# Kernel tuning notes

Hardware: AMD Instinct MI355X
Metric: run time of the kernel (lower is better)

Reference implementation:

```python
import jax, jax.numpy as jnp
import numpy as np

T, B, E, H = 2048, 2, 1024, 16
D = E // H  # head_dim = 64


def setup_inputs() -> dict:
    key = jax.random.key(0)
    ks = jax.random.split(key, 5)
    s = 1.0 / np.sqrt(E)  # keep projections well-scaled like xavier init
    return {
        "query": jax.random.normal(ks[0], (T, B, E), jnp.float32),
        "Wq": jax.random.normal(ks[1], (E, E), jnp.float32) * s,
        "bq": jnp.zeros((E,), jnp.float32),
        "Wk": jax.random.normal(ks[2], (E, E), jnp.float32) * s,
        "bk": jnp.zeros((E,), jnp.float32),
        "Wv": jax.random.normal(ks[3], (E, E), jnp.float32) * s,
        "bv": jnp.zeros((E,), jnp.float32),
        "Wo": jax.random.normal(ks[4], (E, E), jnp.float32) * s,
        "bo": jnp.zeros((E,), jnp.float32),
    }


def reference(query, Wq, bq, Wk, bk, Wv, bv, Wo, bo):
    # query: [T, B, E] (seq_len, batch, embed_dim), fairseq layout
    scaling = D ** -0.5
    q = (query @ Wq.T + bq) * scaling           # [T, B, E]
    k = query @ Wk.T + bk                       # [T, B, E] (self-attention)
    v = query @ Wv.T + bv                       # [T, B, E]
    # split heads: [T, B, H, D]
    q = q.reshape(T, B, H, D)
    k = k.reshape(T, B, H, D)
    v = v.reshape(T, B, H, D)
    # attention scores [B, H, T, S] (S == T, no masks, global window)
    scores = jnp.einsum("tbhd,sbhd->bhts", q, k)
    probs = jax.nn.softmax(scores, axis=-1)     # dropout p=0 -> identity
    attn = jnp.einsum("bhts,sbhd->tbhd", probs, v).reshape(T, B, E)
    return attn @ Wo.T + bo                     # [T, B, E]
```

## Files before the change

### kernel.cpp

```cpp
#include <hip/hip_runtime.h>
#include <hip/hip_bf16.h>
#include <stdint.h>


#define T_SEQ 2048
#define BATCH 2
#define EMB   1024
#define NH    16
#define HD    64

typedef short s16;
typedef s16   bf16x8 __attribute__((ext_vector_type(8)));
typedef float f32x4  __attribute__((ext_vector_type(4)));

__device__ __forceinline__ f32x4 mfma16(bf16x8 a, bf16x8 b, f32x4 c) {
  return __builtin_amdgcn_mfma_f32_16x16x32_bf16(a, b, c, 0, 0, 0);
}

__device__ __forceinline__ void gload16(const void* g, void* l) {
  __builtin_amdgcn_global_load_lds(
      (const __attribute__((address_space(1))) uint32_t*)g,
      (__attribute__((address_space(3))) uint32_t*)l, 16, 0, 0);
}

__device__ __forceinline__ s16 f2b(float x) {
  return (s16)__builtin_bit_cast(unsigned short, __float2bfloat16(x));
}
__device__ __forceinline__ uint32_t pack2(float lo, float hi) {
  return ((uint32_t)(uint16_t)__builtin_bit_cast(unsigned short, __float2bfloat16(hi)) << 16)
       |  (uint32_t)(uint16_t)__builtin_bit_cast(unsigned short, __float2bfloat16(lo));
}

__device__ __forceinline__ bf16x8 cvt8(const float* p) {
  f32x4 a = *(const f32x4*)p;
  f32x4 b = *(const f32x4*)(p + 4);
  bf16x8 r;
  r[0] = f2b(a[0]); r[1] = f2b(a[1]); r[2] = f2b(a[2]); r[3] = f2b(a[3]);
  r[4] = f2b(b[0]); r[5] = f2b(b[1]); r[6] = f2b(b[2]); r[7] = f2b(b[3]);
  return r;
}

__global__ __launch_bounds__(256)
void gemm_qkv_kernel(const float* __restrict__ X,
                     const float* __restrict__ Wq, const float* __restrict__ bq,
                     const float* __restrict__ Wk, const float* __restrict__ bk,
                     const float* __restrict__ Wv, const float* __restrict__ bv,
                     __hip_bfloat16* __restrict__ Qh, __hip_bfloat16* __restrict__ Kh,
                     s16* __restrict__ Vt)
{
  __shared__ __align__(16) s16 lA[128 * 32];
  __shared__ __align__(16) s16 lB[128 * 32];
  const int tid  = threadIdx.x;
  const int lane = tid & 63;
  const int wave = tid >> 6;
  const int which = blockIdx.y >> 3;
  const float* W = (which == 0) ? Wq : (which == 1) ? Wk : Wv;
  const float* bias = (which == 0) ? bq : (which == 1) ? bk : bv;
  const int m0 = blockIdx.x * 128;
  const int n0 = (blockIdx.y & 7) * 128;
  const int srow = tid >> 2;
  const int scol = (tid & 3) * 8;
  const int wr = (wave >> 1) * 64;
  const int wc = (wave & 1) * 64;
  const int fr = lane & 15;
  const int fk = (lane >> 4) * 8;

  f32x4 acc[4][4] = {};

  for (int k0 = 0; k0 < EMB; k0 += 32) {
    bf16x8 a0 = cvt8(X + (size_t)(m0 + srow) * EMB + k0 + scol);
    bf16x8 a1 = cvt8(X + (size_t)(m0 + 64 + srow) * EMB + k0 + scol);
    bf16x8 b0 = cvt8(W + (size_t)(n0 + srow) * EMB + k0 + scol);
    bf16x8 b1 = cvt8(W + (size_t)(n0 + 64 + srow) * EMB + k0 + scol);
    *(bf16x8*)&lA[srow * 32 + scol] = a0;
    *(bf16x8*)&lA[(64 + srow) * 32 + scol] = a1;
    *(bf16x8*)&lB[srow * 32 + scol] = b0;
    *(bf16x8*)&lB[(64 + srow) * 32 + scol] = b1;
    __syncthreads();
    bf16x8 af[4], bfr[4];
#pragma unroll
    for (int i = 0; i < 4; ++i) af[i]  = *(const bf16x8*)&lA[(wr + i * 16 + fr) * 32 + fk];
#pragma unroll
    for (int i = 0; i < 4; ++i) bfr[i] = *(const bf16x8*)&lB[(wc + i * 16 + fr) * 32 + fk];
#pragma unroll
    for (int mi = 0; mi < 4; ++mi)
#pragma unroll
      for (int ni = 0; ni < 4; ++ni)
        acc[mi][ni] = mfma16(af[mi], bfr[ni], acc[mi][ni]);
    __syncthreads();
  }

  const float scale = (which == 0) ? 0.125f * 1.44269504088896f : 1.0f;
  __hip_bfloat16* Y = (which == 0) ? Qh : Kh;
  const int fq = lane >> 4;
#pragma unroll
  for (int mi = 0; mi < 4; ++mi) {
#pragma unroll
    for (int ni = 0; ni < 4; ++ni) {
      const int nn = n0 + wc + ni * 16 + fr;
      const float bb = bias[nn];
      const int h = nn >> 6, d = nn & 63;
#pragma unroll
      for (int r = 0; r < 4; ++r) {
        const int m = m0 + wr + mi * 16 + fq * 4 + r;
        const int t = m >> 1, b = m & 1;
        const float y = (acc[mi][ni][r] + bb) * scale;
        if (which == 2) {
          const int tl = t & 31;
          const int tp = ((tl & 12) << 1) + (tl & 3) + ((tl >> 4) << 2);
          Vt[(((size_t)b * NH + h) * HD + d) * T_SEQ + (t & ~31) + tp] = f2b(y);
        } else {
          Y[(((size_t)b * NH + h) * T_SEQ + t) * HD + d] = __float2bfloat16(y);
        }
      }
    }
  }
}

__global__ __launch_bounds__(256)
void gemm_out_kernel(const s16* __restrict__ X,
                     const float* __restrict__ W,
                     const float* __restrict__ bias,
                     float* __restrict__ Y)
{
  __shared__ __align__(16) s16 lA[128 * 32];
  __shared__ __align__(16) s16 lB[128 * 32];
  const int tid  = threadIdx.x;
  const int lane = tid & 63;
  const int wave = tid >> 6;
  const int m0 = blockIdx.x * 128;
  const int n0 = blockIdx.y * 128;
  const int srow = tid >> 2;
  const int scol = (tid & 3) * 8;
  const int wr = (wave >> 1) * 64;
  const int wc = (wave & 1) * 64;
  const int fr = lane & 15;
  const int fk = (lane >> 4) * 8;

  f32x4 acc[4][4] = {};

  for (int k0 = 0; k0 < EMB; k0 += 32) {
    gload16(X + (size_t)(m0 + srow) * EMB + k0 + scol,      &lA[srow * 32 + scol]);
    gload16(X + (size_t)(m0 + 64 + srow) * EMB + k0 + scol, &lA[(64 + srow) * 32 + scol]);
    bf16x8 b0 = cvt8(W + (size_t)(n0 + srow) * EMB + k0 + scol);
    bf16x8 b1 = cvt8(W + (size_t)(n0 + 64 + srow) * EMB + k0 + scol);
    *(bf16x8*)&lB[srow * 32 + scol] = b0;
    *(bf16x8*)&lB[(64 + srow) * 32 + scol] = b1;
    __syncthreads();
    bf16x8 af[4], bfr[4];
#pragma unroll
    for (int i = 0; i < 4; ++i) af[i]  = *(const bf16x8*)&lA[(wr + i * 16 + fr) * 32 + fk];
#pragma unroll
    for (int i = 0; i < 4; ++i) bfr[i] = *(const bf16x8*)&lB[(wc + i * 16 + fr) * 32 + fk];
#pragma unroll
    for (int mi = 0; mi < 4; ++mi)
#pragma unroll
      for (int ni = 0; ni < 4; ++ni)
        acc[mi][ni] = mfma16(af[mi], bfr[ni], acc[mi][ni]);
    __syncthreads();
  }

  const int fq = lane >> 4;
#pragma unroll
  for (int mi = 0; mi < 4; ++mi) {
#pragma unroll
    for (int ni = 0; ni < 4; ++ni) {
      const int nn = n0 + wc + ni * 16 + fr;
      const float bb = bias[nn];
#pragma unroll
      for (int r = 0; r < 4; ++r) {
        const int m = m0 + wr + mi * 16 + fq * 4 + r;
        Y[(size_t)m * EMB + nn] = acc[mi][ni][r] + bb;
      }
    }
  }
}

__global__ __launch_bounds__(256, 4)
void attn_kernel(const s16* __restrict__ Qh,
                 const s16* __restrict__ Kh,
                 const s16* __restrict__ Vt,
                 __hip_bfloat16* __restrict__ attn)
{
  __shared__ __align__(16) s16 lK[2][64 * 64];
  __shared__ __align__(16) s16 lV[2][64 * 64];
  const int tid  = threadIdx.x;
  const int lane = tid & 63;
  const int wave = tid >> 6;

  const int lid = blockIdx.x;
  const int nid = (lid & 7) * 128 + (lid >> 3);
  const int qb = nid & 31;
  const int bh = nid >> 5;

  const int q0 = qb * 64 + wave * 16;
  const size_t baseK = (size_t)bh * T_SEQ * HD;
  const size_t baseV = (size_t)bh * HD * T_SEQ;
  const int fr = lane & 15;
  const int fq = lane >> 4;
  const int fk = fq * 8;
  const int xk = fr & 7;

  const int srow  = tid >> 3;
  const int scol  = (tid & 7) * 8;
  const int scolK = (((tid & 7) ^ ((tid >> 3) & 7)) * 8);

  const bf16x8 qf0 = *(const bf16x8*)&Qh[baseK + (size_t)(q0 + fr) * HD + fk];
  const bf16x8 qf1 = *(const bf16x8*)&Qh[baseK + (size_t)(q0 + fr) * HD + 32 + fk];

  float m_run = -INFINITY, l_run = 0.f;
  f32x4 o_acc[4] = {};

  auto stage = [&](int b, int sB) {
    gload16(Kh + baseK + (size_t)(sB + srow) * HD + scolK,         &lK[b][srow * 64 + scol]);
    gload16(Kh + baseK + (size_t)(sB + 32 + srow) * HD + scolK,    &lK[b][(32 + srow) * 64 + scol]);
    gload16(Vt + baseV + (size_t)srow * T_SEQ + sB + scolK,        &lV[b][srow * 64 + scol]);
    gload16(Vt + baseV + (size_t)(32 + srow) * T_SEQ + sB + scolK, &lV[b][(32 + srow) * 64 + scol]);
  };

  stage(0, 0);

  for (int t = 0; t < T_SEQ / 64; ++t) {
    const int cur = t & 1;
    __syncthreads();
    if (t + 1 < T_SEQ / 64) stage(cur ^ 1, (t + 1) * 64);

    const s16* kb = lK[cur];
    const s16* vb = lV[cur];

    f32x4 s_acc[4];
#pragma unroll
    for (int sc = 0; sc < 4; ++sc) {
      const int row = (sc * 16 + fr) * 64;
      bf16x8 kf0 = *(const bf16x8*)&kb[row + ((fq ^ xk) << 3)];
      bf16x8 kf1 = *(const bf16x8*)&kb[row + (((fq + 4) ^ xk) << 3)];
      f32x4 z = {};
      z = mfma16(kf0, qf0, z);
      z = mfma16(kf1, qf1, z);
      s_acc[sc] = z;
    }

    bf16x8 vf[2][4];
#pragma unroll
    for (int h = 0; h < 2; ++h)
#pragma unroll
      for (int dn = 0; dn < 4; ++dn)
        vf[h][dn] = *(const bf16x8*)&vb[(dn * 16 + fr) * 64 + (((h * 4 + fq) ^ xk) << 3)];

    float vmax = fmaxf(fmaxf(s_acc[0][0], s_acc[0][1]), fmaxf(s_acc[0][2], s_acc[0][3]));
#pragma unroll
    for (int sc = 1; sc < 4; ++sc)
      vmax = fmaxf(vmax, fmaxf(fmaxf(s_acc[sc][0], s_acc[sc][1]),
                               fmaxf(s_acc[sc][2], s_acc[sc][3])));
    vmax = fmaxf(vmax, __shfl_xor(vmax, 16));
    vmax = fmaxf(vmax, __shfl_xor(vmax, 32));

    if (__any(vmax > m_run + 8.0f)) {
      const float mn = fmaxf(m_run, vmax);
      const float sc_f = __builtin_amdgcn_exp2f(m_run - mn);
      m_run = mn;
      l_run *= sc_f;
      float scb[4];
#pragma unroll
      for (int r = 0; r < 4; ++r) scb[r] = __shfl(sc_f, fq * 20 + r);
#pragma unroll
      for (int dn = 0; dn < 4; ++dn)
#pragma unroll
        for (int r = 0; r < 4; ++r) o_acc[dn][r] *= scb[r];
    }

    float rsum = 0.f;
#pragma unroll
    for (int sc = 0; sc < 4; ++sc)
#pragma unroll
      for (int r = 0; r < 4; ++r) {
        const float p = __builtin_amdgcn_exp2f(s_acc[sc][r] - m_run);
        s_acc[sc][r] = p;
        rsum += p;
      }
    rsum += __shfl_xor(rsum, 16);
    rsum += __shfl_xor(rsum, 32);
    l_run += rsum;

    uint32_t w[4][2];
#pragma unroll
    for (int sc = 0; sc < 4; ++sc) {
      w[sc][0] = pack2(s_acc[sc][0], s_acc[sc][1]);
      w[sc][1] = pack2(s_acc[sc][2], s_acc[sc][3]);
    }
#pragma unroll
    for (int h = 0; h < 2; ++h) {
      union { uint32_t u[4]; bf16x8 v; } pa;
      pa.u[0] = w[2 * h][0];     pa.u[1] = w[2 * h][1];
      pa.u[2] = w[2 * h + 1][0]; pa.u[3] = w[2 * h + 1][1];
#pragma unroll
      for (int dn = 0; dn < 4; ++dn)
        o_acc[dn] = mfma16(pa.v, vf[h][dn], o_acc[dn]);
    }
  }

  const int b = bh >> 4, h = bh & 15;
  float linv[4];
#pragma unroll
  for (int r = 0; r < 4; ++r) linv[r] = 1.0f / __shfl(l_run, fq * 20 + r);
#pragma unroll
  for (int r = 0; r < 4; ++r) {
    const int t = q0 + fq * 4 + r;
#pragma unroll
    for (int dn = 0; dn < 4; ++dn) {
      const int d = dn * 16 + fr;
      attn[((size_t)t * BATCH + b) * EMB + h * HD + d] =
          __float2bfloat16(o_acc[dn][r] * linv[r]);
    }
  }
}

extern "C" void kernel_launch(void* const* d_in, const int* in_sizes, int n_in,
                              void* d_out, int out_size, void* d_ws, size_t ws_size,
                              hipStream_t stream) {
  const float* query = (const float*)d_in[0];
  const float* Wq = (const float*)d_in[1];
  const float* bq = (const float*)d_in[2];
  const float* Wk = (const float*)d_in[3];
  const float* bk = (const float*)d_in[4];
  const float* Wv = (const float*)d_in[5];
  const float* bv = (const float*)d_in[6];
  const float* Wo = (const float*)d_in[7];
  const float* bo = (const float*)d_in[8];

  char* ws = (char*)d_ws;
  const size_t SZ = (size_t)BATCH * NH * T_SEQ * HD * sizeof(s16);
  __hip_bfloat16* Qh = (__hip_bfloat16*)(ws);
  __hip_bfloat16* Kh = (__hip_bfloat16*)(ws + SZ);
  __hip_bfloat16* attnb = (__hip_bfloat16*)(ws + 2 * SZ);
  s16* Vt = (s16*)(ws + 3 * SZ);

  dim3 blk(256);
  gemm_qkv_kernel<<<dim3(32, 24), blk, 0, stream>>>(query, Wq, bq, Wk, bk, Wv, bv, Qh, Kh, Vt);
  attn_kernel<<<dim3(1024), blk, 0, stream>>>((const s16*)Qh, (const s16*)Kh, Vt, attnb);
  gemm_out_kernel<<<dim3(32, 8), blk, 0, stream>>>((const s16*)attnb, Wo, bo, (float*)d_out);
}
```

Before: 148.8 us.

## Pre-convert inputs to bf16 and use direct-to-LDS loads in QKV GEMM

Adds a separate kernel that converts the fp32 query and Wq/Wk/Wv to bf16 once, writing into the output buffer as scratch. The QKV GEMM then loads bf16 tiles straight into LDS with global_load_lds instead of loading fp32, converting and storing per tile. This removes the repeated fp32 reads and conversions across GEMM blocks, at the cost of an extra kernel launch and a full conversion pass. The attention kernel also raises wave priority around its MFMA sections with s_setprio.

```diff
diff --git a/kernel.cpp b/kernel.cpp
--- a/kernel.cpp
+++ b/kernel.cpp
@@ -8,6 +8,8 @@
 #define EMB   1024
 #define NH    16
 #define HD    64
+#define N_X   (T_SEQ * BATCH * EMB)
+#define N_W   (EMB * EMB)
 
 typedef short s16;
 typedef s16   bf16x8 __attribute__((ext_vector_type(8)));
@@ -41,10 +43,28 @@
 }
 
 __global__ __launch_bounds__(256)
-void gemm_qkv_kernel(const float* __restrict__ X,
-                     const float* __restrict__ Wq, const float* __restrict__ bq,
-                     const float* __restrict__ Wk, const float* __restrict__ bk,
-                     const float* __restrict__ Wv, const float* __restrict__ bv,
+void convert_kernel(const float* __restrict__ X, const float* __restrict__ Wq,
+                    const float* __restrict__ Wk, const float* __restrict__ Wv,
+                    s16* __restrict__ dst)
+{
+  const int idx = (blockIdx.x * 256 + threadIdx.x) * 8;
+  const float* src;
+  int off;
+  if (idx < N_X) { src = X; off = idx; }
+  else {
+    const int r = idx - N_X;
+    const int w = r >> 20;
+    src = (w == 0) ? Wq : (w == 1) ? Wk : Wv;
+    off = r & (N_W - 1);
+  }
+  *(bf16x8*)&dst[idx] = cvt8(src + off);
+}
+
+__global__ __launch_bounds__(256)
+void gemm_qkv_kernel(const s16* __restrict__ Xb,
+                     const s16* __restrict__ Wb,
+                     const float* __restrict__ bq, const float* __restrict__ bk,
+                     const float* __restrict__ bv,
                      __hip_bfloat16* __restrict__ Qh, __hip_bfloat16* __restrict__ Kh,
                      s16* __restrict__ Vt)
 {
@@ -54,7 +74,7 @@
   const int lane = tid & 63;
   const int wave = tid >> 6;
   const int which = blockIdx.y >> 3;
-  const float* W = (which == 0) ? Wq : (which == 1) ? Wk : Wv;
+  const s16* W = Wb + (size_t)which * N_W;
   const float* bias = (which == 0) ? bq : (which == 1) ? bk : bv;
   const int m0 = blockIdx.x * 128;
   const int n0 = (blockIdx.y & 7) * 128;
@@ -68,14 +88,10 @@
   f32x4 acc[4][4] = {};
 
   for (int k0 = 0; k0 < EMB; k0 += 32) {
-    bf16x8 a0 = cvt8(X + (size_t)(m0 + srow) * EMB + k0 + scol);
-    bf16x8 a1 = cvt8(X + (size_t)(m0 + 64 + srow) * EMB + k0 + scol);
-    bf16x8 b0 = cvt8(W + (size_t)(n0 + srow) * EMB + k0 + scol);
-    bf16x8 b1 = cvt8(W + (size_t)(n0 + 64 + srow) * EMB + k0 + scol);
-    *(bf16x8*)&lA[srow * 32 + scol] = a0;
-    *(bf16x8*)&lA[(64 + srow) * 32 + scol] = a1;
-    *(bf16x8*)&lB[srow * 32 + scol] = b0;
-    *(bf16x8*)&lB[(64 + srow) * 32 + scol] = b1;
+    gload16(Xb + (size_t)(m0 + srow) * EMB + k0 + scol,      &lA[srow * 32 + scol]);
+    gload16(Xb + (size_t)(m0 + 64 + srow) * EMB + k0 + scol, &lA[(64 + srow) * 32 + scol]);
+    gload16(W + (size_t)(n0 + srow) * EMB + k0 + scol,       &lB[srow * 32 + scol]);
+    gload16(W + (size_t)(n0 + 64 + srow) * EMB + k0 + scol,  &lB[(64 + srow) * 32 + scol]);
     __syncthreads();
     bf16x8 af[4], bfr[4];
 #pragma unroll
@@ -229,6 +245,7 @@
     const s16* vb = lV[cur];
 
     f32x4 s_acc[4];
+    __builtin_amdgcn_s_setprio(1);
 #pragma unroll
     for (int sc = 0; sc < 4; ++sc) {
       const int row = (sc * 16 + fr) * 64;
@@ -239,6 +256,7 @@
       z = mfma16(kf1, qf1, z);
       s_acc[sc] = z;
     }
+    __builtin_amdgcn_s_setprio(0);
 
     bf16x8 vf[2][4];
 #pragma unroll
@@ -288,6 +306,7 @@
       w[sc][0] = pack2(s_acc[sc][0], s_acc[sc][1]);
       w[sc][1] = pack2(s_acc[sc][2], s_acc[sc][3]);
     }
+    __builtin_amdgcn_s_setprio(1);
 #pragma unroll
     for (int h = 0; h < 2; ++h) {
       union { uint32_t u[4]; bf16x8 v; } pa;
@@ -297,6 +316,7 @@
       for (int dn = 0; dn < 4; ++dn)
         o_acc[dn] = mfma16(pa.v, vf[h][dn], o_acc[dn]);
     }
+    __builtin_amdgcn_s_setprio(0);
   }
 
   const int b = bh >> 4, h = bh & 15;
@@ -335,8 +355,12 @@
   __hip_bfloat16* attnb = (__hip_bfloat16*)(ws + 2 * SZ);
   s16* Vt = (s16*)(ws + 3 * SZ);
 
+  s16* Xb = (s16*)d_out;
+  s16* Wb = Xb + (size_t)N_X;
+
   dim3 blk(256);
-  gemm_qkv_kernel<<<dim3(32, 24), blk, 0, stream>>>(query, Wq, bq, Wk, bk, Wv, bv, Qh, Kh, Vt);
+  convert_kernel<<<dim3((N_X + 3 * N_W) / (256 * 8)), blk, 0, stream>>>(query, Wq, Wk, Wv, Xb);
+  gemm_qkv_kernel<<<dim3(32, 24), blk, 0, stream>>>(Xb, Wb, bq, bk, bv, Qh, Kh, Vt);
   attn_kernel<<<dim3(1024), blk, 0, stream>>>((const s16*)Qh, (const s16*)Kh, Vt, attnb);
   gemm_out_kernel<<<dim3(32, 8), blk, 0, stream>>>((const s16*)attnb, Wo, bo, (float*)d_out);
 }
```

Result: faster. 140.4 us (-5.6%).
